# Kernel tuning notes

Hardware: AMD Instinct MI355X
Metric: run time of the kernel (lower is better)

Reference implementation:

```python
import jax, jax.numpy as jnp
import numpy as np

N, F, D, C, K, E, M = 50000, 512, 128, 128, 3, 20000, 8  # nodes, feat, emb, conv, cheb K, hyperedges, edge size
EPS = 1e-5


def setup_inputs() -> dict:
    key = jax.random.key(0)
    ks = jax.random.split(key, 9)
    pos_set = jax.random.normal(ks[0], (N, F), jnp.float32)
    # each hyperedge = M distinct nodes (contiguous window => distinct, like the original expansion assumes)
    base = jax.random.randint(ks[1], (E, 1), 0, N - M)
    members = (base + jnp.arange(M, dtype=jnp.int32)[None, :]).astype(jnp.int32)  # [E, M]
    # expansion(): full directed clique (no self loops) on the E*M duplicated entries
    row, col = np.where(~np.eye(M, dtype=bool))            # M*(M-1) intra-edge pairs
    offs = np.arange(E, dtype=np.int64)[:, None] * M
    edge_index = jnp.asarray(np.stack([(offs + row[None, :]).ravel(),
                                       (offs + col[None, :]).ravel()]), jnp.int32)  # [2, E*M*(M-1)]
    batch = jnp.asarray(np.repeat(np.arange(E, dtype=np.int64), M), jnp.int32)      # [E*M]
    W_enc = jax.random.normal(ks[2], (F, D), jnp.float32) / np.float32(np.sqrt(F))
    b_enc = jnp.zeros((D,), jnp.float32)
    gn_gamma = 1.0 + 0.1 * jax.random.normal(ks[3], (D,), jnp.float32)
    gn_beta = 0.01 * jax.random.normal(ks[4], (D,), jnp.float32)
    gn_alpha = 1.0 + 0.1 * jax.random.normal(ks[5], (D,), jnp.float32)
    cheb_W = jax.random.normal(ks[6], (K, D, C), jnp.float32) / np.float32(np.sqrt(D * K))
    cheb_b = jnp.zeros((C,), jnp.float32)
    lin_W = jax.random.normal(ks[7], (2 * C, 1), jnp.float32) / np.float32(np.sqrt(2 * C))
    lin_b = jnp.zeros((1,), jnp.float32)
    return dict(pos_set=pos_set, W_enc=W_enc, b_enc=b_enc, gn_gamma=gn_gamma, gn_beta=gn_beta,
                gn_alpha=gn_alpha, cheb_W=cheb_W, cheb_b=cheb_b, lin_W=lin_W, lin_b=lin_b,
                members=members, edge_index=edge_index, batch=batch)


def reference(pos_set, W_enc, b_enc, gn_gamma, gn_beta, gn_alpha, cheb_W, cheb_b,
              lin_W, lin_b, members, edge_index, batch):
    num_entries = E * M
    # running_type == 'structure': Hardtanh(Linear(feature))
    x = jnp.clip(pos_set @ W_enc + b_enc, -1.0, 1.0)                    # [N, D]
    # partition(): duplicate node features per (node, hyperedge) incidence
    xe = x[members.reshape(-1)]                                         # [E*M, D]
    # GraphNorm (per-hyperedge group): out = gamma*(x - alpha*mean)/sqrt(var+eps) + beta
    cnt = jax.ops.segment_sum(jnp.ones((num_entries,), xe.dtype), batch, num_segments=E)  # [E]
    mean = jax.ops.segment_sum(xe, batch, num_segments=E) / cnt[:, None]
    ctr = xe - gn_alpha * mean[batch]
    var = jax.ops.segment_sum(ctr * ctr, batch, num_segments=E) / cnt[:, None]
    xe = gn_gamma * ctr / jnp.sqrt(var + EPS)[batch] + gn_beta
    # AlphaDropout is identity at eval time
    # ChebConv: sym norm, lambda_max=2 => L_hat = -D^{-1/2} A D^{-1/2} (zero diagonal)
    src, dst = edge_index[0], edge_index[1]
    deg = jax.ops.segment_sum(jnp.ones_like(src, dtype=xe.dtype), dst, num_segments=num_entries)
    w = -jax.lax.rsqrt(deg[src] * deg[dst])                             # [nE] scaled-Laplacian weights

    def Lhat(h):  # sparse matvec via gather + segment scatter-add
        return jax.ops.segment_sum(w[:, None] * h[src], dst, num_segments=num_entries)

    Tx0 = xe
    Tx1 = Lhat(Tx0)
    out = Tx0 @ cheb_W[0] + Tx1 @ cheb_W[1]
    Tkm1, Tkm2 = Tx1, Tx0
    for k in range(2, K):  # K is a small static constant
        Tk = 2.0 * Lhat(Tkm1) - Tkm2
        out = out + Tk @ cheb_W[k]
        Tkm1, Tkm2 = Tk, Tkm1
    h = jnp.clip(out + cheb_b, -1.0, 1.0)                               # Hardtanh
    # poolings per hyperedge
    y_max = jax.ops.segment_max(h, batch, num_segments=E)
    y_min = jax.ops.segment_min(h, batch, num_segments=E)
    y_norm = jnp.sqrt(jax.ops.segment_sum(h * h, batch, num_segments=E) / cnt[:, None])
    y = jnp.concatenate([y_max - y_min, y_norm], axis=1)                # [E, 2C]
    logits = y @ lin_W + lin_b
    return jax.nn.sigmoid(logits).squeeze(-1)                           # [E] link probabilities
```

## Files before the change

kernel.cpp:

```cpp
#include <hip/hip_runtime.h>
#include <hip/hip_bf16.h>

#define NN   50000
#define FF   512
#define DD   128
#define CC   128
#define EE   20000
#define MM   8
#define EPSV 1e-5f

typedef __attribute__((ext_vector_type(8)))  short bfrag;
typedef __attribute__((ext_vector_type(4)))  unsigned int u32x4;
typedef __attribute__((ext_vector_type(16))) float f32x16;

__device__ __forceinline__ f32x16 mfma32(u32x4 a, u32x4 b, f32x16 c) {
    return __builtin_amdgcn_mfma_f32_32x32x16_bf16(
        __builtin_bit_cast(bfrag, a), __builtin_bit_cast(bfrag, b), c, 0, 0, 0);
}

__device__ __forceinline__ unsigned short f2bf(float f) {
    unsigned u = __builtin_bit_cast(unsigned, f);
    unsigned r = u + 0x7FFFu + ((u >> 16) & 1u);
    return (unsigned short)(r >> 16);
}
__device__ __forceinline__ float bf2f(unsigned short h) {
    unsigned u = ((unsigned)h) << 16;
    return __builtin_bit_cast(float, u);
}
__device__ __forceinline__ void split1(float a, short& hi, short& lo) {
    unsigned short h = f2bf(a);
    hi = (short)h;
    lo = (short)f2bf(a - bf2f(h));
}

template <int CTRL>
__device__ __forceinline__ float dpp_addstep(float x) {
    const int xi = __builtin_bit_cast(int, x);
    const int yi = __builtin_amdgcn_update_dpp(xi, xi, CTRL, 0xF, 0xF, true);
    return x + __builtin_bit_cast(float, yi);
}
__device__ __forceinline__ float sum8(float x) {
    x = dpp_addstep<0xB1>(x);
    x = dpp_addstep<0x4E>(x);
    x = dpp_addstep<0x141>(x);
    return x;
}

__device__ __forceinline__ void pack_split8(const float* v, u32x4& hi, u32x4& lo) {
#pragma unroll
    for (int p = 0; p < 4; p++) {
        const unsigned u0 = __builtin_bit_cast(unsigned, v[2 * p]);
        const unsigned u1 = __builtin_bit_cast(unsigned, v[2 * p + 1]);
        const unsigned h0 = u0 & 0xFFFF0000u, h1 = u1 & 0xFFFF0000u;
        hi[p] = (u0 >> 16) | h1;
        const float r0 = v[2 * p]     - __builtin_bit_cast(float, h0);
        const float r1 = v[2 * p + 1] - __builtin_bit_cast(float, h1);
        unsigned lp;
        asm("v_cvt_pk_bf16_f32 %0, %1, %2" : "=v"(lp) : "v"(r0), "v"(r1));
        lo[p] = lp;
    }
}
__device__ __forceinline__ void pack8(const float* v, u32x4& w) {
#pragma unroll
    for (int p = 0; p < 4; p++) {
        unsigned lp;
        asm("v_cvt_pk_bf16_f32 %0, %1, %2" : "=v"(lp) : "v"(v[2 * p]), "v"(v[2 * p + 1]));
        w[p] = lp;
    }
}

__global__ void prep_kernel(const float* __restrict__ W_enc,
                            const float* __restrict__ cheb_W,
                            unsigned short* __restrict__ Ep_hi,
                            unsigned short* __restrict__ Ep_lo,
                            unsigned short* __restrict__ Wp_hi,
                            unsigned short* __restrict__ Wp_lo) {
    const int tid = blockIdx.x * blockDim.x + threadIdx.x;
    const int stride = gridDim.x * blockDim.x;
    for (int p = tid; p < 64 * 128; p += stride) {
        const int slot = p >> 7, n = p & 127;
        bfrag fh, fl;
#pragma unroll
        for (int j = 0; j < 8; j++) {
            const float v = W_enc[(size_t)(slot * 8 + j) * DD + n];
            short h, lo; split1(v, h, lo);
            fh[j] = h; fl[j] = lo;
        }
        *(bfrag*)&Ep_hi[(size_t)p * 8] = fh;
        *(bfrag*)&Ep_lo[(size_t)p * 8] = fl;
    }
    const float c1 = 1.0f / 7.0f;
    const float c2 = -47.0f / 49.0f;
    const float c3 = -1.0f / 7.0f;
    const float c4 = 12.0f / 49.0f;
    for (int p = tid; p < 32 * 128; p += stride) {
        const int slot = p >> 7, c = p & 127;
        bfrag fh, fl;
#pragma unroll
        for (int j = 0; j < 8; j++) {
            const int k = slot * 8 + j;
            float v;
            if (k < DD) {
                v = cheb_W[0 * DD * CC + k * CC + c]
                  + c1 * cheb_W[1 * DD * CC + k * CC + c]
                  + c2 * cheb_W[2 * DD * CC + k * CC + c];
            } else {
                const int d = k - DD;
                v = c3 * cheb_W[1 * DD * CC + d * CC + c]
                  + c4 * cheb_W[2 * DD * CC + d * CC + c];
            }
            short h, lo; split1(v, h, lo);
            fh[j] = h; fl[j] = lo;
        }
        *(bfrag*)&Wp_hi[(size_t)p * 8] = fh;
        *(bfrag*)&Wp_lo[(size_t)p * 8] = fl;
    }
}

__global__ __launch_bounds__(256, 4) void enc_kernel(
        const float* __restrict__ pos,
        const unsigned short* __restrict__ Ep_hi,
        const unsigned short* __restrict__ Ep_lo,
        const float* __restrict__ b_enc,
        float* __restrict__ x) {
    const int t = threadIdx.x;
    const int w = t >> 6, l = t & 63, l31 = l & 31, lg2 = l >> 5;

    int arow = blockIdx.x * 32 + l31;
    if (arow >= NN) arow = NN - 1;
    const float* aBase = pos + (size_t)arow * FF;

    f32x16 acc;
#pragma unroll
    for (int i = 0; i < 16; i++) acc[i] = 0.f;

    for (int ks = 0; ks < 32; ks++) {
        const int koff = ks * 16 + lg2 * 8;
        const float4 a0 = *(const float4*)(aBase + koff);
        const float4 a1 = *(const float4*)(aBase + koff + 4);
        const float av[8] = {a0.x, a0.y, a0.z, a0.w, a1.x, a1.y, a1.z, a1.w};
        u32x4 ahi, alo;
        pack_split8(av, ahi, alo);

        const int slot = ks * 2 + lg2;
        const size_t boff = ((size_t)slot * 128 + w * 32 + l31) * 8;
        const u32x4 bhi = *(const u32x4*)(Ep_hi + boff);
        const u32x4 blo = *(const u32x4*)(Ep_lo + boff);
        acc = mfma32(ahi, bhi, acc);
        acc = mfma32(ahi, blo, acc);
        acc = mfma32(alo, bhi, acc);
    }

    const int col = w * 32 + l31;
    const float bias = b_enc[col];
    const int brow = blockIdx.x * 32;
#pragma unroll
    for (int r = 0; r < 16; r++) {
        const int row = brow + (r & 3) + 8 * (r >> 2) + 4 * lg2;
        if (row < NN) {
            const float v = acc[r] + bias;
            x[(size_t)row * DD + col] = fminf(1.0f, fmaxf(-1.0f, v));
        }
    }
}

__global__ __launch_bounds__(256, 4) void edge_kernel(
        const float* __restrict__ x,
        const int* __restrict__ members,
        const unsigned short* __restrict__ Wp_hi,
        const unsigned short* __restrict__ Wp_lo,
        const float* __restrict__ gn_gamma,
        const float* __restrict__ gn_beta,
        const float* __restrict__ gn_alpha,
        const float* __restrict__ cheb_b,
        const float* __restrict__ lin_W,
        const float* __restrict__ lin_b,
        float* __restrict__ out) {
    const int t = threadIdx.x;
    const int w = t >> 6, l = t & 63, l31 = l & 31, lg2 = l >> 5;

    const int node = members[blockIdx.x * 128 + w * 32 + l31];
    const float* xrow = x + (size_t)node * DD;

    f32x16 acc[4];
#pragma unroll
    for (int nt = 0; nt < 4; nt++)
#pragma unroll
        for (int i = 0; i < 16; i++) acc[nt][i] = 0.f;

    for (int ks = 0; ks < 8; ks++) {
        const int koff = ks * 16 + lg2 * 8;
        const float4 a0 = *(const float4*)(xrow + koff);
        const float4 a1 = *(const float4*)(xrow + koff + 4);
        float v[8] = {a0.x, a0.y, a0.z, a0.w, a1.x, a1.y, a1.z, a1.w};

        float s[8];
#pragma unroll
        for (int j = 0; j < 8; j++) s[j] = sum8(v[j]);

        {
            const float4 al0 = *(const float4*)(gn_alpha + koff);
            const float4 al1 = *(const float4*)(gn_alpha + koff + 4);
            const float al[8] = {al0.x, al0.y, al0.z, al0.w, al1.x, al1.y, al1.z, al1.w};
#pragma unroll
            for (int j = 0; j < 8; j++) {
                const float m = s[j] * 0.125f;
                v[j] = v[j] - al[j] * m;
                s[j] = m * (1.0f - al[j]);
            }
        }
        float t2[8];
#pragma unroll
        for (int j = 0; j < 8; j++) t2[j] = sum8(v[j] * v[j]);

        float nv[8], sv[8];
        {
            const float4 g0 = *(const float4*)(gn_gamma + koff);
            const float4 g1 = *(const float4*)(gn_gamma + koff + 4);
            const float4 b0 = *(const float4*)(gn_beta + koff);
            const float4 b1 = *(const float4*)(gn_beta + koff + 4);
            const float gm[8] = {g0.x, g0.y, g0.z, g0.w, g1.x, g1.y, g1.z, g1.w};
            const float bt[8] = {b0.x, b0.y, b0.z, b0.w, b1.x, b1.y, b1.z, b1.w};
#pragma unroll
            for (int j = 0; j < 8; j++) {
                const float sc = gm[j] * rsqrtf(t2[j] * 0.125f + EPSV);
                nv[j] = sc * v[j] + bt[j];
                sv[j] = 8.0f * (sc * s[j] + bt[j]);
            }
        }
        u32x4 ahi, alo, shi;
        pack_split8(nv, ahi, alo);
        pack8(sv, shi);

        const int slotN = ks * 2 + lg2;
        const int slotS = 16 + slotN;
#pragma unroll
        for (int nt = 0; nt < 4; nt++) {
            const int col = nt * 32 + l31;
            const size_t offN = ((size_t)slotN * 128 + col) * 8;
            const size_t offS = ((size_t)slotS * 128 + col) * 8;
            const u32x4 wahi = *(const u32x4*)(Wp_hi + offN);
            const u32x4 walo = *(const u32x4*)(Wp_lo + offN);
            const u32x4 wbh  = *(const u32x4*)(Wp_hi + offS);
            acc[nt] = mfma32(ahi, wahi, acc[nt]);
            acc[nt] = mfma32(ahi, walo, acc[nt]);
            acc[nt] = mfma32(alo, wahi, acc[nt]);
            acc[nt] = mfma32(shi, wbh,  acc[nt]);
        }
    }

    float p[4] = {0.f, 0.f, 0.f, 0.f};
#pragma unroll
    for (int nt = 0; nt < 4; nt++) {
        const int col = nt * 32 + l31;
        const float bias = cheb_b[col];
        const float w1 = lin_W[col], w2 = lin_W[DD + col];
#pragma unroll
        for (int e = 0; e < 4; e++) {
            float mx = -2.f, mn = 2.f, ssq = 0.f;
#pragma unroll
            for (int q = 0; q < 4; q++) {
                float h = acc[nt][e * 4 + q] + bias;
                h = fminf(1.0f, fmaxf(-1.0f, h));
                mx = fmaxf(mx, h); mn = fminf(mn, h); ssq += h * h;
            }
            mx = fmaxf(mx, __shfl_xor(mx, 32));
            mn = fminf(mn, __shfl_xor(mn, 32));
            ssq += __shfl_xor(ssq, 32);
            p[e] += (mx - mn) * w1 + sqrtf(ssq * 0.125f) * w2;
        }
    }
#pragma unroll
    for (int mk = 1; mk <= 16; mk <<= 1)
#pragma unroll
        for (int e = 0; e < 4; e++) p[e] += __shfl_xor(p[e], mk);
    if (l == 0) {
        const float b0 = lin_b[0];
#pragma unroll
        for (int e = 0; e < 4; e++) {
            const float z = p[e] + b0;
            out[blockIdx.x * 16 + w * 4 + e] = 1.0f / (1.0f + expf(-z));
        }
    }
}

extern "C" void kernel_launch(void* const* d_in, const int* in_sizes, int n_in,
                              void* d_out, int out_size, void* d_ws, size_t ws_size,
                              hipStream_t stream) {
    const float* pos    = (const float*)d_in[0];
    const float* W_enc  = (const float*)d_in[1];
    const float* b_enc  = (const float*)d_in[2];
    const float* gammaP = (const float*)d_in[3];
    const float* betaP  = (const float*)d_in[4];
    const float* alphaP = (const float*)d_in[5];
    const float* cheb_W = (const float*)d_in[6];
    const float* cheb_b = (const float*)d_in[7];
    const float* lin_W  = (const float*)d_in[8];
    const float* lin_b  = (const float*)d_in[9];
    const int*   members = (const int*)d_in[10];
    float* out = (float*)d_out;

    char* ws = (char*)d_ws;
    float* x = (float*)ws;
    unsigned short* Ep_hi = (unsigned short*)(ws + 25600000);
    unsigned short* Ep_lo = Ep_hi + 64 * 128 * 8;
    unsigned short* Wp_hi = Ep_lo + 64 * 128 * 8;
    unsigned short* Wp_lo = Wp_hi + 32 * 128 * 8;

    prep_kernel<<<32, 256, 0, stream>>>(W_enc, cheb_W, Ep_hi, Ep_lo, Wp_hi, Wp_lo);
    enc_kernel<<<(NN + 31) / 32, 256, 0, stream>>>(pos, Ep_hi, Ep_lo, b_enc, x);
    edge_kernel<<<EE / 16, 256, 0, stream>>>(x, members, Wp_hi, Wp_lo,
                                             gammaP, betaP, alphaP, cheb_b, lin_W, lin_b, out);
}
```

Measured before the change: 287.1 us.

## Widen encoder wave tiles, prefetch A rows, fuse group-norm stat reductions

The encoder kernel now runs two waves per block, each computing two 32-column tiles. Each loaded and bf16-split A fragment is reused across twice as many MFMAs, instead of four waves each reloading and converting the same rows. Both the encoder and edge kernels gain a two-stage register prefetch of the next A fragments to hide global load latency. The edge kernel computes mean and sum of squares in one pass, using interleaved DPP add steps, and derives the variance algebraically. This removes a dependent second reduction, at some cost in numerical stability and register pressure.

```diff
diff --git a/kernel.cpp b/kernel.cpp
--- a/kernel.cpp
+++ b/kernel.cpp
@@ -117,7 +117,7 @@
     }
 }
 
-__global__ __launch_bounds__(256, 4) void enc_kernel(
+__global__ __launch_bounds__(128, 4) void enc_kernel(
         const float* __restrict__ pos,
         const unsigned short* __restrict__ Ep_hi,
         const unsigned short* __restrict__ Ep_lo,
@@ -128,38 +128,62 @@
 
     int arow = blockIdx.x * 32 + l31;
     if (arow >= NN) arow = NN - 1;
-    const float* aBase = pos + (size_t)arow * FF;
-
-    f32x16 acc;
-#pragma unroll
-    for (int i = 0; i < 16; i++) acc[i] = 0.f;
-
-    for (int ks = 0; ks < 32; ks++) {
-        const int koff = ks * 16 + lg2 * 8;
-        const float4 a0 = *(const float4*)(aBase + koff);
-        const float4 a1 = *(const float4*)(aBase + koff + 4);
+    const float* aBase = pos + (size_t)arow * FF + lg2 * 8;
+
+    f32x16 acc[2];
+#pragma unroll
+    for (int ntl = 0; ntl < 2; ntl++)
+#pragma unroll
+        for (int i = 0; i < 16; i++) acc[ntl][i] = 0.f;
+
+    auto body = [&](float4 a0, float4 a1, int ks) {
         const float av[8] = {a0.x, a0.y, a0.z, a0.w, a1.x, a1.y, a1.z, a1.w};
         u32x4 ahi, alo;
         pack_split8(av, ahi, alo);
-
         const int slot = ks * 2 + lg2;
-        const size_t boff = ((size_t)slot * 128 + w * 32 + l31) * 8;
-        const u32x4 bhi = *(const u32x4*)(Ep_hi + boff);
-        const u32x4 blo = *(const u32x4*)(Ep_lo + boff);
-        acc = mfma32(ahi, bhi, acc);
-        acc = mfma32(ahi, blo, acc);
-        acc = mfma32(alo, bhi, acc);
-    }
-
-    const int col = w * 32 + l31;
-    const float bias = b_enc[col];
+#pragma unroll
+        for (int ntl = 0; ntl < 2; ntl++) {
+            const int col = w * 64 + ntl * 32 + l31;
+            const size_t boff = ((size_t)slot * 128 + col) * 8;
+            const u32x4 bhi = *(const u32x4*)(Ep_hi + boff);
+            const u32x4 blo = *(const u32x4*)(Ep_lo + boff);
+            acc[ntl] = mfma32(ahi, bhi, acc[ntl]);
+            acc[ntl] = mfma32(ahi, blo, acc[ntl]);
+            acc[ntl] = mfma32(alo, bhi, acc[ntl]);
+        }
+    };
+
+    float4 pa0 = *(const float4*)(aBase);
+    float4 pa1 = *(const float4*)(aBase + 4);
+    float4 pb0 = *(const float4*)(aBase + 16);
+    float4 pb1 = *(const float4*)(aBase + 20);
+    for (int ks = 0; ks < 32; ks += 2) {
+        const float4 c0 = pa0, c1 = pa1;
+        if (ks + 2 < 32) {
+            pa0 = *(const float4*)(aBase + (ks + 2) * 16);
+            pa1 = *(const float4*)(aBase + (ks + 2) * 16 + 4);
+        }
+        body(c0, c1, ks);
+        const float4 d0 = pb0, d1 = pb1;
+        if (ks + 3 < 32) {
+            pb0 = *(const float4*)(aBase + (ks + 3) * 16);
+            pb1 = *(const float4*)(aBase + (ks + 3) * 16 + 4);
+        }
+        body(d0, d1, ks + 1);
+    }
+
     const int brow = blockIdx.x * 32;
 #pragma unroll
-    for (int r = 0; r < 16; r++) {
-        const int row = brow + (r & 3) + 8 * (r >> 2) + 4 * lg2;
-        if (row < NN) {
-            const float v = acc[r] + bias;
-            x[(size_t)row * DD + col] = fminf(1.0f, fmaxf(-1.0f, v));
+    for (int ntl = 0; ntl < 2; ntl++) {
+        const int col = w * 64 + ntl * 32 + l31;
+        const float bias = b_enc[col];
+#pragma unroll
+        for (int r = 0; r < 16; r++) {
+            const int row = brow + (r & 3) + 8 * (r >> 2) + 4 * lg2;
+            if (row < NN) {
+                const float v = acc[ntl][r] + bias;
+                x[(size_t)row * DD + col] = fminf(1.0f, fmaxf(-1.0f, v));
+            }
         }
     }
 }
@@ -180,7 +204,7 @@
     const int w = t >> 6, l = t & 63, l31 = l & 31, lg2 = l >> 5;
 
     const int node = members[blockIdx.x * 128 + w * 32 + l31];
-    const float* xrow = x + (size_t)node * DD;
+    const float* xrow = x + (size_t)node * DD + lg2 * 8;
 
     f32x16 acc[4];
 #pragma unroll
@@ -188,45 +212,43 @@
 #pragma unroll
         for (int i = 0; i < 16; i++) acc[nt][i] = 0.f;
 
-    for (int ks = 0; ks < 8; ks++) {
+    auto body = [&](float4 a0, float4 a1, int ks) {
         const int koff = ks * 16 + lg2 * 8;
-        const float4 a0 = *(const float4*)(xrow + koff);
-        const float4 a1 = *(const float4*)(xrow + koff + 4);
-        float v[8] = {a0.x, a0.y, a0.z, a0.w, a1.x, a1.y, a1.z, a1.w};
-
-        float s[8];
-#pragma unroll
-        for (int j = 0; j < 8; j++) s[j] = sum8(v[j]);
-
-        {
-            const float4 al0 = *(const float4*)(gn_alpha + koff);
-            const float4 al1 = *(const float4*)(gn_alpha + koff + 4);
-            const float al[8] = {al0.x, al0.y, al0.z, al0.w, al1.x, al1.y, al1.z, al1.w};
-#pragma unroll
-            for (int j = 0; j < 8; j++) {
-                const float m = s[j] * 0.125f;
-                v[j] = v[j] - al[j] * m;
-                s[j] = m * (1.0f - al[j]);
-            }
-        }
-        float t2[8];
-#pragma unroll
-        for (int j = 0; j < 8; j++) t2[j] = sum8(v[j] * v[j]);
+        const float4 al0 = *(const float4*)(gn_alpha + koff);
+        const float4 al1 = *(const float4*)(gn_alpha + koff + 4);
+        const float4 g0  = *(const float4*)(gn_gamma + koff);
+        const float4 g1  = *(const float4*)(gn_gamma + koff + 4);
+        const float4 b0  = *(const float4*)(gn_beta + koff);
+        const float4 b1  = *(const float4*)(gn_beta + koff + 4);
+        const float al[8] = {al0.x, al0.y, al0.z, al0.w, al1.x, al1.y, al1.z, al1.w};
+        const float gm[8] = {g0.x, g0.y, g0.z, g0.w, g1.x, g1.y, g1.z, g1.w};
+        const float bt[8] = {b0.x, b0.y, b0.z, b0.w, b1.x, b1.y, b1.z, b1.w};
+
+        const float v[8] = {a0.x, a0.y, a0.z, a0.w, a1.x, a1.y, a1.z, a1.w};
+        float s[8], q[8];
+#pragma unroll
+        for (int j = 0; j < 8; j++) { s[j] = v[j]; q[j] = v[j] * v[j]; }
+#pragma unroll
+        for (int j = 0; j < 8; j++) s[j] = dpp_addstep<0xB1>(s[j]);
+#pragma unroll
+        for (int j = 0; j < 8; j++) q[j] = dpp_addstep<0xB1>(q[j]);
+#pragma unroll
+        for (int j = 0; j < 8; j++) s[j] = dpp_addstep<0x4E>(s[j]);
+#pragma unroll
+        for (int j = 0; j < 8; j++) q[j] = dpp_addstep<0x4E>(q[j]);
+#pragma unroll
+        for (int j = 0; j < 8; j++) s[j] = dpp_addstep<0x141>(s[j]);
+#pragma unroll
+        for (int j = 0; j < 8; j++) q[j] = dpp_addstep<0x141>(q[j]);
 
         float nv[8], sv[8];
-        {
-            const float4 g0 = *(const float4*)(gn_gamma + koff);
-            const float4 g1 = *(const float4*)(gn_gamma + koff + 4);
-            const float4 b0 = *(const float4*)(gn_beta + koff);
-            const float4 b1 = *(const float4*)(gn_beta + koff + 4);
-            const float gm[8] = {g0.x, g0.y, g0.z, g0.w, g1.x, g1.y, g1.z, g1.w};
-            const float bt[8] = {b0.x, b0.y, b0.z, b0.w, b1.x, b1.y, b1.z, b1.w};
-#pragma unroll
-            for (int j = 0; j < 8; j++) {
-                const float sc = gm[j] * rsqrtf(t2[j] * 0.125f + EPSV);
-                nv[j] = sc * v[j] + bt[j];
-                sv[j] = 8.0f * (sc * s[j] + bt[j]);
-            }
+#pragma unroll
+        for (int j = 0; j < 8; j++) {
+            const float m   = s[j] * 0.125f;
+            const float var = q[j] * 0.125f - al[j] * (2.0f - al[j]) * m * m;
+            const float sc  = gm[j] * rsqrtf(var + EPSV);
+            nv[j] = sc * (v[j] - al[j] * m) + bt[j];
+            sv[j] = 8.0f * (sc * m * (1.0f - al[j]) + bt[j]);
         }
         u32x4 ahi, alo, shi;
         pack_split8(nv, ahi, alo);
@@ -247,6 +269,25 @@
             acc[nt] = mfma32(alo, wahi, acc[nt]);
             acc[nt] = mfma32(shi, wbh,  acc[nt]);
         }
+    };
+
+    float4 pa0 = *(const float4*)(xrow);
+    float4 pa1 = *(const float4*)(xrow + 4);
+    float4 pb0 = *(const float4*)(xrow + 16);
+    float4 pb1 = *(const float4*)(xrow + 20);
+    for (int ks = 0; ks < 8; ks += 2) {
+        const float4 c0 = pa0, c1 = pa1;
+        if (ks + 2 < 8) {
+            pa0 = *(const float4*)(xrow + (ks + 2) * 16);
+            pa1 = *(const float4*)(xrow + (ks + 2) * 16 + 4);
+        }
+        body(c0, c1, ks);
+        const float4 d0 = pb0, d1 = pb1;
+        if (ks + 3 < 8) {
+            pb0 = *(const float4*)(xrow + (ks + 3) * 16);
+            pb1 = *(const float4*)(xrow + (ks + 3) * 16 + 4);
+        }
+        body(d0, d1, ks + 1);
     }
 
     float p[4] = {0.f, 0.f, 0.f, 0.f};
@@ -259,8 +300,8 @@
         for (int e = 0; e < 4; e++) {
             float mx = -2.f, mn = 2.f, ssq = 0.f;
 #pragma unroll
-            for (int q = 0; q < 4; q++) {
-                float h = acc[nt][e * 4 + q] + bias;
+            for (int q2 = 0; q2 < 4; q2++) {
+                float h = acc[nt][e * 4 + q2] + bias;
                 h = fminf(1.0f, fmaxf(-1.0f, h));
                 mx = fmaxf(mx, h); mn = fminf(mn, h); ssq += h * h;
             }
@@ -308,7 +349,7 @@
     unsigned short* Wp_lo = Wp_hi + 32 * 128 * 8;
 
     prep_kernel<<<32, 256, 0, stream>>>(W_enc, cheb_W, Ep_hi, Ep_lo, Wp_hi, Wp_lo);
-    enc_kernel<<<(NN + 31) / 32, 256, 0, stream>>>(pos, Ep_hi, Ep_lo, b_enc, x);
+    enc_kernel<<<(NN + 31) / 32, 128, 0, stream>>>(pos, Ep_hi, Ep_lo, b_enc, x);
     edge_kernel<<<EE / 16, 256, 0, stream>>>(x, members, Wp_hi, Wp_lo,
                                              gammaP, betaP, alphaP, cheb_b, lin_W, lin_b, out);
 }
```

Result: no change. 291.0 us (+1.4%).
